# Optimization experiments

Measured on AMD Instinct MI355X. Metric: run time of the kernel, lower is better.

Reference implementation:

```python
import jax, jax.numpy as jnp
import numpy as np

B, L, C = 2, 2048, 1024
DK, H = 64, 16

def setup_inputs() -> dict:
    key = jax.random.key(0)
    ks = jax.random.split(key, 12)
    def lin(kw, kb, out_dim, in_dim):
        w = jax.random.normal(kw, (out_dim, in_dim), jnp.float32) * (1.0 / np.sqrt(in_dim))
        b = jnp.zeros((out_dim,), jnp.float32)
        return w, b
    WQ_w, WQ_b = lin(ks[0], ks[1], DK * H, C)
    WK_w, WK_b = lin(ks[2], ks[3], DK * H, C)
    WV_w, WV_b = lin(ks[4], ks[5], DK * H, C)
    WO_w, WO_b = lin(ks[6], ks[7], C, DK * H)
    qx = jax.random.normal(ks[8], (B, L, C), jnp.float32)
    kx = jax.random.normal(ks[9], (B, L, C), jnp.float32)
    vx = jax.random.normal(ks[10], (B, L, C), jnp.float32)
    maskPAD = jax.random.randint(ks[11], (B, L, L), 0, 2, jnp.int32)
    return {"qx": qx, "kx": kx, "vx": vx, "maskPAD": maskPAD,
            "WQ_w": WQ_w, "WQ_b": WQ_b, "WK_w": WK_w, "WK_b": WK_b,
            "WV_w": WV_w, "WV_b": WV_b, "WO_w": WO_w, "WO_b": WO_b}

def reference(qx, kx, vx, maskPAD, WQ_w, WQ_b, WK_w, WK_b, WV_w, WV_b, WO_w, WO_b):
    Bq, qL, _ = qx.shape
    kvL = kx.shape[1]
    # projections -> [B, H, L, DK]
    q = (qx @ WQ_w.T + WQ_b).reshape(Bq, qL, H, DK).transpose(0, 2, 1, 3)
    k = (kx @ WK_w.T + WK_b).reshape(Bq, kvL, H, DK).transpose(0, 2, 1, 3)
    v = (vx @ WV_w.T + WV_b).reshape(Bq, kvL, H, DK).transpose(0, 2, 1, 3)
    scores = jnp.einsum('bhqd,bhkd->bhqk', q, k) / np.sqrt(DK).astype(np.float32)
    scores = jnp.where((maskPAD == 0)[:, None, :, :], jnp.float32(-2**15 + 1), scores)
    alpha = jax.nn.softmax(scores, axis=3)  # dropout p=0 (eval)
    z = jnp.einsum('bhqk,bhkd->bhqd', alpha, v)
    z = z.transpose(0, 2, 1, 3).reshape(Bq, qL, H * DK)
    return z @ WO_w.T + WO_b
```

## Files before the change

### kernel.cpp

```cpp
#include <hip/hip_runtime.h>
#include <stdint.h>
#include <math.h>

typedef short short8 __attribute__((ext_vector_type(8)));
typedef short short4v __attribute__((ext_vector_type(4)));
typedef float float4v __attribute__((ext_vector_type(4)));
typedef float float2v __attribute__((ext_vector_type(2)));

static __device__ __forceinline__ float bf2f(uint16_t u) {
    union { uint32_t i; float f; } x; x.i = ((uint32_t)u) << 16; return x.f;
}
static __device__ __forceinline__ uint16_t f2bf(float f) {
    union { float f; uint32_t i; } x; x.f = f;
    uint32_t u = x.i;
    u += 0x7FFFu + ((u >> 16) & 1u);
    return (uint16_t)(u >> 16);
}
static __device__ __forceinline__ uint16_t f2bf_sane(float f) {
    uint16_t u = f2bf(f);
    if ((u & 0x7F80u) == 0x7F80u) u = 0;
    return u;
}
static __device__ __forceinline__ float san_f32(float f) {
    union { float f; uint32_t i; } x; x.f = f;
    if (((x.i >> 23) & 0xFFu) == 0xFFu) return 0.f;
    return x.f;
}
static __device__ __forceinline__ void gll16(const void* g, void* l) {
    __builtin_amdgcn_global_load_lds((const __attribute__((address_space(1))) void*)g,
                                     (__attribute__((address_space(3))) void*)l,
                                     16, 0, 0);
}
static __device__ __forceinline__ short8 load8(const void* p, size_t off, int fp32) {
    if (!fp32) return *(const short8*)((const uint16_t*)p + off);
    const float* f = (const float*)p + off;
    const float4v a = *(const float4v*)f;
    const float4v b = *(const float4v*)(f + 4);
    short8 r;
    r[0] = (short)f2bf(a[0]); r[1] = (short)f2bf(a[1]);
    r[2] = (short)f2bf(a[2]); r[3] = (short)f2bf(a[3]);
    r[4] = (short)f2bf(b[0]); r[5] = (short)f2bf(b[1]);
    r[6] = (short)f2bf(b[2]); r[7] = (short)f2bf(b[3]);
    return r;
}

static __device__ __forceinline__ float fexp2(float x) {
#if __has_builtin(__builtin_amdgcn_exp2f)
    return __builtin_amdgcn_exp2f(x);
#else
    float r; asm("v_exp_f32 %0, %1\ns_nop 0" : "=v"(r) : "v"(x)); return r;
#endif
}

static __device__ __forceinline__ float maskexp2(float s, uint32_t nib, int r) {
    union { float f; uint32_t u; } x; x.f = s;
    const uint32_t keep = (uint32_t)(((int32_t)(nib << (31 - r))) >> 31);
    x.u = (x.u & keep) | (~keep & 0xFF800000u);
    return fexp2(x.f);
}

static __device__ __forceinline__ float4v mfma16_bf16(short4v a, short4v b, float4v c) {
#if __has_builtin(__builtin_amdgcn_mfma_f32_16x16x16bf16_1k)
    return __builtin_amdgcn_mfma_f32_16x16x16bf16_1k(a, b, c, 0, 0, 0);
#else
    float4v d = c;
    asm volatile("v_mfma_f32_16x16x16_bf16 %0, %1, %2, %0"
                 : "+v"(d) : "v"(a), "v"(b));
    return d;
#endif
}

__global__ __launch_bounds__(256) void detect_kernel(const uint16_t* qx, int* flag)
{
    __shared__ int s;
    const int tid = threadIdx.x;
    if (tid == 0) s = 0;
    __syncthreads();
    int bad = 0;
#pragma unroll 8
    for (int i = 0; i < 64; ++i) {
        const uint16_t u = qx[tid * 64 + i];
        bad |= ((u & 0x7F80u) == 0x7F80u) ? 1 : 0;
    }
    if (bad) atomicOr(&s, 1);
    __syncthreads();
    if (tid == 0) *flag = s;
}

__global__ __launch_bounds__(256) void pack_kernel(
    const int* __restrict__ mask, uint64_t* __restrict__ mask64)
{
    const int wave = threadIdx.x >> 6, lane = threadIdx.x & 63;
    const int row = blockIdx.x * 4 + wave;
    const int* src = mask + (size_t)row * 2048;
#pragma unroll 4
    for (int j = 0; j < 32; ++j) {
        const int m = src[j * 64 + lane];
        const uint64_t bal = __ballot(m != 0);
        if (lane == 0) mask64[(size_t)row * 32 + j] = bal;
    }
}

__global__ __launch_bounds__(256) void convert_kernel(
    const void* qx, const void* kx, const void* vx,
    const void* wq, const void* wk, const void* wv, const void* wo,
    const void* bq, const void* bk, const void* bv, const void* bo,
    uint16_t* cIn, uint16_t* cW, uint16_t* cB, const int* flag)
{
    const int mode = *flag;
    if (!mode) return;
    const int z = blockIdx.z;
    if (z < 3) {
        const void* src = (z == 0) ? qx : (z == 1) ? kx : vx;
        uint16_t* dst = cIn + (size_t)z * 4194304;
#pragma unroll
        for (int it = 0; it < 8; ++it) {
            const int idx8 = (blockIdx.x * 8 + it) * 256 + threadIdx.x;
            *(short8*)(dst + (size_t)idx8 * 8) = load8(src, (size_t)idx8 * 8, 1);
        }
    } else if (z < 7) {
        const int t = z - 3;
        const void* src = (t == 0) ? wq : (t == 1) ? wk : (t == 2) ? wv : wo;
        uint16_t* dst = cW + (size_t)t * 1048576;
#pragma unroll
        for (int it = 0; it < 2; ++it) {
            const int idx8 = (blockIdx.x * 2 + it) * 256 + threadIdx.x;
            *(short8*)(dst + (size_t)idx8 * 8) = load8(src, (size_t)idx8 * 8, 1);
        }
    } else {
        const int idx8 = blockIdx.x * 256 + threadIdx.x;
        if (idx8 < 128) {
#pragma unroll
            for (int t = 0; t < 4; ++t) {
                const void* src = (t == 0) ? bq : (t == 1) ? bk : (t == 2) ? bv : bo;
                *(short8*)(cB + t * 1024 + idx8 * 8) = load8(src, (size_t)idx8 * 8, 1);
            }
        }
    }
}

template <int MI, int NI>
static __device__ __forceinline__ void gemm_tile(
    const uint16_t* __restrict__ A, const uint16_t* __restrict__ W,
    const uint16_t* __restrict__ bias, void* __restrict__ C,
    int c_fp32, float out_scale)
{
    constexpr int TM = MI * 32, TN = NI * 32;
    __shared__ __align__(16) uint16_t sA[TM * 32];
    __shared__ __align__(16) uint16_t sB[TN * 32];

    const int tid  = threadIdx.x;
    const int wave = tid >> 6;
    const int lane = tid & 63;
    const int quad = lane >> 4;
    const int l15  = lane & 15;
    const int m0 = blockIdx.y * TM;
    const int n0 = blockIdx.x * TN;
    const int wm = (wave >> 1) * (MI * 16);
    const int wn = (wave & 1) * (NI * 16);
    const int r16 = lane >> 2;
    const int ch  = lane & 3;

    float4v acc[MI][NI] = {};

    for (int k0 = 0; k0 < 1024; k0 += 32) {
        __syncthreads();
#pragma unroll
        for (int g = wave; g < TM / 16; g += 4)
            gll16(A + (size_t)(m0 + g * 16 + r16) * 1024 + k0 + ch * 8,
                  (char*)sA + (size_t)g * 1024);
#pragma unroll
        for (int g = wave; g < TN / 16; g += 4)
            gll16(W + (size_t)(n0 + g * 16 + r16) * 1024 + k0 + ch * 8,
                  (char*)sB + (size_t)g * 1024);
        asm volatile("s_waitcnt vmcnt(0)" ::: "memory");
        __syncthreads();

        short8 af[MI], bfr[NI];
#pragma unroll
        for (int i = 0; i < MI; ++i)
            af[i] = *(const short8*)&sA[(wm + i * 16 + l15) * 32 + quad * 8];
#pragma unroll
        for (int j = 0; j < NI; ++j)
            bfr[j] = *(const short8*)&sB[(wn + j * 16 + l15) * 32 + quad * 8];
#pragma unroll
        for (int mi = 0; mi < MI; ++mi)
#pragma unroll
            for (int ni = 0; ni < NI; ++ni)
                acc[mi][ni] = __builtin_amdgcn_mfma_f32_16x16x32_bf16(
                    af[mi], bfr[ni], acc[mi][ni], 0, 0, 0);
    }

#pragma unroll
    for (int ni = 0; ni < NI; ++ni) {
        const int n = n0 + wn + ni * 16 + l15;
        const float bv = bf2f(bias[n]);
#pragma unroll
        for (int mi = 0; mi < MI; ++mi) {
            const int mbase = m0 + wm + mi * 16 + quad * 4;
#pragma unroll
            for (int r = 0; r < 4; ++r) {
                const float v = (acc[mi][ni][r] + bv) * out_scale;
                const size_t idx = (size_t)(mbase + r) * 1024 + n;
                if (c_fp32) ((float*)C)[idx] = san_f32(v);
                else        ((uint16_t*)C)[idx] = f2bf_sane(v);
            }
        }
    }
}

__global__ __launch_bounds__(256) void qkv_kernel(
    const uint16_t* rqx, const uint16_t* rkx, const uint16_t* rvx,
    const uint16_t* rwq, const uint16_t* rwk, const uint16_t* rwv,
    const uint16_t* rbq, const uint16_t* rbk, const uint16_t* rbv,
    const uint16_t* cIn, const uint16_t* cW, const uint16_t* cB,
    uint16_t* Q, uint16_t* K, uint16_t* V, const int* flag)
{
    const int mode = *flag;
    const int z = blockIdx.z;
    const uint16_t* A = mode ? cIn + (size_t)z * 4194304
                             : ((z == 0) ? rqx : (z == 1) ? rkx : rvx);
    const uint16_t* W = mode ? cW + (size_t)z * 1048576
                             : ((z == 0) ? rwq : (z == 1) ? rwk : rwv);
    const uint16_t* b = mode ? cB + z * 1024
                             : ((z == 0) ? rbq : (z == 1) ? rbk : rbv);
    uint16_t* C = (z == 0) ? Q : (z == 1) ? K : V;
    const float sc = (z == 0) ? 0.18033688f : 1.0f;
    gemm_tile<4, 4>(A, W, b, C, 0, sc);
}

__global__ __launch_bounds__(256) void out_kernel(
    const uint16_t* Z, const uint16_t* rwo, const uint16_t* rbo,
    const uint16_t* cW, const uint16_t* cB, void* out, const int* flag)
{
    const int mode = *flag;
    const uint16_t* W = mode ? cW + 3 * 1048576 : rwo;
    const uint16_t* b = mode ? cB + 3 * 1024 : rbo;
    gemm_tile<2, 4>(Z, W, b, out, mode, 1.0f);
}

__global__ __launch_bounds__(256) void vtrans_kernel(
    const uint16_t* __restrict__ Vp, uint16_t* __restrict__ Vt)
{
    __shared__ __align__(16) uint16_t t[64][72];
    const int tid = threadIdx.x;
    const int lt = blockIdx.x, h = blockIdx.y, b = blockIdx.z;
#pragma unroll
    for (int p = 0; p < 2; ++p) {
        const int r = p * 32 + (tid >> 3);
        const int c = (tid & 7) * 8;
        *(short8*)&t[r][c] =
            *(const short8*)(Vp + (size_t)(b * 2048 + lt * 64 + r) * 1024 + h * 64 + c);
    }
    __syncthreads();
#pragma unroll
    for (int p = 0; p < 2; ++p) {
        const int d = p * 32 + (tid >> 3);
        const int c = (tid & 7) * 8;
        short8 v;
#pragma unroll
        for (int j = 0; j < 8; ++j) v[j] = (short)t[c + j][d];
        *(short8*)(Vt + (size_t)((b * 16 + h) * 64 + d) * 2048 + lt * 64 + c) = v;
    }
}

#define VS 72

__global__ __launch_bounds__(256, 4) void attn_kernel(
    const uint16_t* __restrict__ Q, const uint16_t* __restrict__ Kp,
    const uint16_t* __restrict__ Vt, const uint64_t* __restrict__ mask64,
    uint16_t* __restrict__ Oa, uint16_t* __restrict__ Ob,
    float* __restrict__ lpart)
{
    __shared__ __align__(16) uint16_t sK[64 * VS];
    __shared__ __align__(16) uint16_t sV[64 * VS];

    const int tid = threadIdx.x;
    const int wave = tid >> 6, lane = tid & 63;
    const int quad = lane >> 4, l15 = lane & 15;
    const int qt = blockIdx.x, h = blockIdx.y;
    const int b = blockIdx.z & 1, half = blockIdx.z >> 1;
    const int q0 = qt * 128;
    const int qw = q0 + wave * 32;

    const int srow = tid >> 2;
    const int sc0  = tid & 3;

    short8 qf[2][2];
#pragma unroll
    for (int mi = 0; mi < 2; ++mi)
#pragma unroll
        for (int kk = 0; kk < 2; ++kk)
            qf[mi][kk] = *(const short8*)(Q + (size_t)(b * 2048 + qw + mi * 16 + l15) * 1024
                                            + h * 64 + (quad + 4 * kk) * 8);

    const uint64_t* mrow[2];
#pragma unroll
    for (int mj = 0; mj < 2; ++mj)
        mrow[mj] = mask64 + (size_t)(b * 2048 + qw + mj * 16 + l15) * 32;

    float4v oaccT[4][2] = {};
    float2v lsum2[2] = {};

    const int kt_lo = half * 16, kt_hi = kt_lo + 16;
    for (int kt = kt_lo; kt < kt_hi; ++kt) {
        const int k0 = kt * 64;
        const short8 kx0 = *(const short8*)(Kp + (size_t)(b * 2048 + k0 + srow) * 1024 + h * 64 + sc0 * 8);
        const short8 kx1 = *(const short8*)(Kp + (size_t)(b * 2048 + k0 + srow) * 1024 + h * 64 + (sc0 + 4) * 8);
        const short8 vx0 = *(const short8*)(Vt + (size_t)((b * 16 + h) * 64 + srow) * 2048 + k0 + sc0 * 8);
        const short8 vx1 = *(const short8*)(Vt + (size_t)((b * 16 + h) * 64 + srow) * 2048 + k0 + (sc0 + 4) * 8);
        const uint64_t mwq0 = mrow[0][kt] >> (quad * 4);
        const uint64_t mwq1 = mrow[1][kt] >> (quad * 4);
        __syncthreads();
        *(short8*)&sK[srow * VS + sc0 * 8]       = kx0;
        *(short8*)&sK[srow * VS + (sc0 + 4) * 8] = kx1;
        *(short8*)&sV[srow * VS + sc0 * 8]       = vx0;
        *(short8*)&sV[srow * VS + (sc0 + 4) * 8] = vx1;
        __syncthreads();

        float4v sacc[2][4] = {};
        __builtin_amdgcn_s_setprio(1);
#pragma unroll
        for (int ni = 0; ni < 4; ++ni) {
            const int row = ni * 16 + l15;
#pragma unroll
            for (int kk = 0; kk < 2; ++kk) {
                const short8 kf = *(const short8*)&sK[row * VS + (quad + 4 * kk) * 8];
                sacc[0][ni] = __builtin_amdgcn_mfma_f32_16x16x32_bf16(kf, qf[0][kk], sacc[0][ni], 0, 0, 0);
                sacc[1][ni] = __builtin_amdgcn_mfma_f32_16x16x32_bf16(kf, qf[1][kk], sacc[1][ni], 0, 0, 0);
            }
        }
        __builtin_amdgcn_s_setprio(0);

        short4v pf[2][4];
#pragma unroll
        for (int mj = 0; mj < 2; ++mj) {
            const uint64_t mwq = mj ? mwq1 : mwq0;
#pragma unroll
            for (int ni = 0; ni < 4; ++ni) {
                const uint32_t nib = (uint32_t)(mwq >> (ni * 16)) & 0xFu;
                const float p0 = maskexp2(sacc[mj][ni][0], nib, 0);
                const float p1 = maskexp2(sacc[mj][ni][1], nib, 1);
                const float p2 = maskexp2(sacc[mj][ni][2], nib, 2);
                const float p3 = maskexp2(sacc[mj][ni][3], nib, 3);
                float2v lo; lo[0] = p0; lo[1] = p1;
                float2v hi; hi[0] = p2; hi[1] = p3;
                lsum2[mj] += lo;
                lsum2[mj] += hi;
                short4v t;
                t[0] = (short)f2bf(p0);
                t[1] = (short)f2bf(p1);
                t[2] = (short)f2bf(p2);
                t[3] = (short)f2bf(p3);
                pf[mj][ni] = t;
            }
        }

        __builtin_amdgcn_s_setprio(1);
#pragma unroll
        for (int di = 0; di < 4; ++di) {
            const int row = di * 16 + l15;
#pragma unroll
            for (int ni = 0; ni < 4; ++ni) {
                const short4v vf = *(const short4v*)&sV[row * VS + ni * 16 + quad * 4];
                oaccT[di][0] = mfma16_bf16(vf, pf[0][ni], oaccT[di][0]);
                oaccT[di][1] = mfma16_bf16(vf, pf[1][ni], oaccT[di][1]);
            }
        }
        __builtin_amdgcn_s_setprio(0);
    }

#if !__has_builtin(__builtin_amdgcn_mfma_f32_16x16x16bf16_1k)
    asm volatile("s_nop 7\ns_nop 7\ns_nop 7" ::: "memory");
#endif

    float lsum[2];
#pragma unroll
    for (int mj = 0; mj < 2; ++mj) lsum[mj] = lsum2[mj][0] + lsum2[mj][1];

#pragma unroll
    for (int mj = 0; mj < 2; ++mj) {
        lsum[mj] += __shfl_xor(lsum[mj], 16);
        lsum[mj] += __shfl_xor(lsum[mj], 32);
    }

    uint16_t* Op = half ? Ob : Oa;
#pragma unroll
    for (int mj = 0; mj < 2; ++mj) {
        const int qrow = qw + mj * 16 + l15;
#pragma unroll
        for (int di = 0; di < 4; ++di) {
            short4v o;
#pragma unroll
            for (int r = 0; r < 4; ++r) o[r] = (short)f2bf(oaccT[di][mj][r]);
            *(short4v*)(Op + (size_t)(b * 2048 + qrow) * 1024 + h * 64 + di * 16 + quad * 4) = o;
        }
        if (quad == 0)
            lpart[half * 65536 + (b * 16 + h) * 2048 + qrow] = lsum[mj];
    }
}

__global__ __launch_bounds__(256) void combine_kernel(
    const uint16_t* __restrict__ Oa, const uint16_t* __restrict__ Ob,
    const float* __restrict__ lpart, uint16_t* __restrict__ Z)
{
    const int e8 = blockIdx.x * 256 + threadIdx.x;
    const int flat = e8 * 8;
    const int bh_row = flat >> 10;
    const int h = (flat >> 6) & 15;
    const int b = bh_row >> 11;
    const int row = bh_row & 2047;
    const int lidx = (b * 16 + h) * 2048 + row;
    const float inv = 1.0f / fmaxf(lpart[lidx] + lpart[65536 + lidx], 1e-37f);
    const short8 a = *(const short8*)(Oa + flat);
    const short8 c = *(const short8*)(Ob + flat);
    short8 o;
#pragma unroll
    for (int j = 0; j < 8; ++j)
        o[j] = (short)f2bf_sane((bf2f((uint16_t)a[j]) + bf2f((uint16_t)c[j])) * inv);
    *(short8*)(Z + flat) = o;
}

extern "C" void kernel_launch(void* const* d_in, const int* in_sizes, int n_in,
                              void* d_out, int out_size, void* d_ws, size_t ws_size,
                              hipStream_t stream)
{
    const void* qx  = d_in[0];
    const void* kx  = d_in[1];
    const void* vx  = d_in[2];
    const int*  msk = (const int*)d_in[3];

    char* ws = (char*)d_ws;
    const size_t MB = 1024 * 1024;
    uint16_t* cIn = (uint16_t*)(ws);
    uint16_t* cW  = (uint16_t*)(ws + 24 * MB);
    uint16_t* cB  = (uint16_t*)(ws + 32 * MB);
    int*      flg = (int*)(ws + 32 * MB + 16 * 1024);
    uint16_t* Qb  = (uint16_t*)(ws + 33 * MB);
    uint16_t* Kb  = (uint16_t*)(ws + 41 * MB);
    uint16_t* Vb  = (uint16_t*)(ws + 49 * MB);
    uint64_t* m64 = (uint64_t*)(ws + 57 * MB);
    uint16_t* Vt  = (uint16_t*)(ws + 8 * MB);
    uint16_t* Oa  = (uint16_t*)(ws);
    uint16_t* Ob  = (uint16_t*)(ws + 16 * MB);
    float*    lp  = (float*)(ws + 49 * MB);
    uint16_t* Zb  = Oa;

    detect_kernel<<<1, 256, 0, stream>>>((const uint16_t*)qx, flg);
    pack_kernel<<<1024, 256, 0, stream>>>(msk, m64);
    convert_kernel<<<dim3(256, 1, 8), 256, 0, stream>>>(
        qx, kx, vx, d_in[4], d_in[6], d_in[8], d_in[10],
        d_in[5], d_in[7], d_in[9], d_in[11], cIn, cW, cB, flg);
    qkv_kernel<<<dim3(8, 32, 3), 256, 0, stream>>>(
        (const uint16_t*)qx, (const uint16_t*)kx, (const uint16_t*)vx,
        (const uint16_t*)d_in[4], (const uint16_t*)d_in[6], (const uint16_t*)d_in[8],
        (const uint16_t*)d_in[5], (const uint16_t*)d_in[7], (const uint16_t*)d_in[9],
        cIn, cW, cB, Qb, Kb, Vb, flg);
    vtrans_kernel<<<dim3(32, 16, 2), 256, 0, stream>>>(Vb, Vt);
    attn_kernel<<<dim3(16, 16, 4), 256, 0, stream>>>(Qb, Kb, Vt, m64, Oa, Ob, lp);
    combine_kernel<<<4096, 256, 0, stream>>>(Oa, Ob, lp, Zb);
    out_kernel<<<dim3(8, 64), 256, 0, stream>>>(
        Zb, (const uint16_t*)d_in[10], (const uint16_t*)d_in[11], cW, cB, d_out, flg);
}
```

Baseline: 303.0 us.

## Split attention KV range into three segments and fold detect into pack kernel

The attention kernel now splits the 32 key tiles into three segments (11/11/10) instead of two halves, launching 1536 blocks instead of 1024 so the GPU is filled more evenly. The combine kernel sums three partial outputs and three partial row sums. Separately, the NaN/Inf detect kernel is merged into the mask pack kernel as an extra block, saving one launch. In exchange it adds another partial-output buffer with its write and read traffic, and it moves the workspace layout (lpart now reuses the 24 MB offset region).

```diff
diff --git a/kernel.cpp b/kernel.cpp
--- a/kernel.cpp
+++ b/kernel.cpp
@@ -70,27 +70,27 @@
 #endif
 }
 
-__global__ __launch_bounds__(256) void detect_kernel(const uint16_t* qx, int* flag)
-{
-    __shared__ int s;
-    const int tid = threadIdx.x;
-    if (tid == 0) s = 0;
-    __syncthreads();
-    int bad = 0;
+__global__ __launch_bounds__(256) void pack_kernel(
+    const int* __restrict__ mask, uint64_t* __restrict__ mask64,
+    const uint16_t* __restrict__ qx, int* __restrict__ flag)
+{
+    const int wave = threadIdx.x >> 6, lane = threadIdx.x & 63;
+    if (blockIdx.x == 1024) {
+        __shared__ int s;
+        const int tid = threadIdx.x;
+        if (tid == 0) s = 0;
+        __syncthreads();
+        int bad = 0;
 #pragma unroll 8
-    for (int i = 0; i < 64; ++i) {
-        const uint16_t u = qx[tid * 64 + i];
-        bad |= ((u & 0x7F80u) == 0x7F80u) ? 1 : 0;
-    }
-    if (bad) atomicOr(&s, 1);
-    __syncthreads();
-    if (tid == 0) *flag = s;
-}
-
-__global__ __launch_bounds__(256) void pack_kernel(
-    const int* __restrict__ mask, uint64_t* __restrict__ mask64)
-{
-    const int wave = threadIdx.x >> 6, lane = threadIdx.x & 63;
+        for (int i = 0; i < 64; ++i) {
+            const uint16_t u = qx[tid * 64 + i];
+            bad |= ((u & 0x7F80u) == 0x7F80u) ? 1 : 0;
+        }
+        if (bad) atomicOr(&s, 1);
+        __syncthreads();
+        if (tid == 0) *flag = s;
+        return;
+    }
     const int row = blockIdx.x * 4 + wave;
     const int* src = mask + (size_t)row * 2048;
 #pragma unroll 4
@@ -270,7 +270,7 @@
     const uint16_t* __restrict__ Q, const uint16_t* __restrict__ Kp,
     const uint16_t* __restrict__ Vt, const uint64_t* __restrict__ mask64,
     uint16_t* __restrict__ Oa, uint16_t* __restrict__ Ob,
-    float* __restrict__ lpart)
+    uint16_t* __restrict__ Oc, float* __restrict__ lpart)
 {
     __shared__ __align__(16) uint16_t sK[64 * VS];
     __shared__ __align__(16) uint16_t sV[64 * VS];
@@ -279,7 +279,7 @@
     const int wave = tid >> 6, lane = tid & 63;
     const int quad = lane >> 4, l15 = lane & 15;
     const int qt = blockIdx.x, h = blockIdx.y;
-    const int b = blockIdx.z & 1, half = blockIdx.z >> 1;
+    const int b = blockIdx.z & 1, seg = blockIdx.z >> 1;
     const int q0 = qt * 128;
     const int qw = q0 + wave * 32;
 
@@ -302,7 +302,8 @@
     float4v oaccT[4][2] = {};
     float2v lsum2[2] = {};
 
-    const int kt_lo = half * 16, kt_hi = kt_lo + 16;
+    const int kt_lo = seg * 11;
+    const int kt_hi = (seg == 2) ? 32 : kt_lo + 11;
     for (int kt = kt_lo; kt < kt_hi; ++kt) {
         const int k0 = kt * 64;
         const short8 kx0 = *(const short8*)(Kp + (size_t)(b * 2048 + k0 + srow) * 1024 + h * 64 + sc0 * 8);
@@ -384,7 +385,7 @@
         lsum[mj] += __shfl_xor(lsum[mj], 32);
     }
 
-    uint16_t* Op = half ? Ob : Oa;
+    uint16_t* Op = (seg == 0) ? Oa : (seg == 1) ? Ob : Oc;
 #pragma unroll
     for (int mj = 0; mj < 2; ++mj) {
         const int qrow = qw + mj * 16 + l15;
@@ -396,13 +397,14 @@
             *(short4v*)(Op + (size_t)(b * 2048 + qrow) * 1024 + h * 64 + di * 16 + quad * 4) = o;
         }
         if (quad == 0)
-            lpart[half * 65536 + (b * 16 + h) * 2048 + qrow] = lsum[mj];
+            lpart[seg * 65536 + (b * 16 + h) * 2048 + qrow] = lsum[mj];
     }
 }
 
 __global__ __launch_bounds__(256) void combine_kernel(
     const uint16_t* __restrict__ Oa, const uint16_t* __restrict__ Ob,
-    const float* __restrict__ lpart, uint16_t* __restrict__ Z)
+    const uint16_t* __restrict__ Oc, const float* __restrict__ lpart,
+    uint16_t* __restrict__ Z)
 {
     const int e8 = blockIdx.x * 256 + threadIdx.x;
     const int flat = e8 * 8;
@@ -411,13 +413,14 @@
     const int b = bh_row >> 11;
     const int row = bh_row & 2047;
     const int lidx = (b * 16 + h) * 2048 + row;
-    const float inv = 1.0f / fmaxf(lpart[lidx] + lpart[65536 + lidx], 1e-37f);
+    const float inv = 1.0f / fmaxf(lpart[lidx] + lpart[65536 + lidx] + lpart[131072 + lidx], 1e-37f);
     const short8 a = *(const short8*)(Oa + flat);
     const short8 c = *(const short8*)(Ob + flat);
+    const short8 d = *(const short8*)(Oc + flat);
     short8 o;
 #pragma unroll
     for (int j = 0; j < 8; ++j)
-        o[j] = (short)f2bf_sane((bf2f((uint16_t)a[j]) + bf2f((uint16_t)c[j])) * inv);
+        o[j] = (short)f2bf_sane((bf2f((uint16_t)a[j]) + bf2f((uint16_t)c[j]) + bf2f((uint16_t)d[j])) * inv);
     *(short8*)(Z + flat) = o;
 }
 
@@ -443,11 +446,11 @@
     uint16_t* Vt  = (uint16_t*)(ws + 8 * MB);
     uint16_t* Oa  = (uint16_t*)(ws);
     uint16_t* Ob  = (uint16_t*)(ws + 16 * MB);
-    float*    lp  = (float*)(ws + 49 * MB);
+    uint16_t* Oc  = (uint16_t*)(ws + 49 * MB);
+    float*    lp  = (float*)(ws + 24 * MB);
     uint16_t* Zb  = Oa;
 
-    detect_kernel<<<1, 256, 0, stream>>>((const uint16_t*)qx, flg);
-    pack_kernel<<<1024, 256, 0, stream>>>(msk, m64);
+    pack_kernel<<<1025, 256, 0, stream>>>(msk, m64, (const uint16_t*)qx, flg);
     convert_kernel<<<dim3(256, 1, 8), 256, 0, stream>>>(
         qx, kx, vx, d_in[4], d_in[6], d_in[8], d_in[10],
         d_in[5], d_in[7], d_in[9], d_in[11], cIn, cW, cB, flg);
@@ -457,8 +460,8 @@
         (const uint16_t*)d_in[5], (const uint16_t*)d_in[7], (const uint16_t*)d_in[9],
         cIn, cW, cB, Qb, Kb, Vb, flg);
     vtrans_kernel<<<dim3(32, 16, 2), 256, 0, stream>>>(Vb, Vt);
-    attn_kernel<<<dim3(16, 16, 4), 256, 0, stream>>>(Qb, Kb, Vt, m64, Oa, Ob, lp);
-    combine_kernel<<<4096, 256, 0, stream>>>(Oa, Ob, lp, Zb);
+    attn_kernel<<<dim3(16, 16, 6), 256, 0, stream>>>(Qb, Kb, Vt, m64, Oa, Ob, Oc, lp);
+    combine_kernel<<<4096, 256, 0, stream>>>(Oa, Ob, Oc, lp, Zb);
     out_kernel<<<dim3(8, 64), 256, 0, stream>>>(
         Zb, (const uint16_t*)d_in[10], (const uint16_t*)d_in[11], cW, cB, d_out, flg);
 }
```

Result: no change. 304.5 us (+0.5%).
